# Optimization experiments

Hardware: AMD Instinct MI355X
Metric: run time of the kernel (lower is better)

## Reference

```python
import jax, jax.numpy as jnp
import numpy as np

B, T, V, Dm = 2, 2048, 32000, 1024
DI, N, R, L, K = 2048, 16, 64, 4, 4  # d_inner, n_states, dt_rank, n_layers, conv kernel


def setup_inputs() -> dict:
    key = jax.random.key(0)
    ks = jax.random.split(key, 10)
    ids = jax.random.randint(ks[0], (B, T), 0, V)

    def nrm(k, shape, s=0.02):
        return jax.random.normal(k, shape, jnp.float32) * s

    embed_W = nrm(ks[1], (V, Dm)).at[0].set(0.0)  # padding_idx=0 row zeroed; tied with output proj
    out_b = jnp.zeros((V,), jnp.float32)
    ln_w = jnp.ones((Dm,), jnp.float32)
    ln_b = jnp.zeros((Dm,), jnp.float32)
    norm_w = jnp.ones((L, Dm), jnp.float32)
    norm_b = jnp.zeros((L, Dm), jnp.float32)
    in_proj_W = nrm(ks[2], (L, 2 * DI, Dm))
    conv_W = nrm(ks[3], (L, DI, K), 0.1)
    conv_b = jnp.zeros((L, DI), jnp.float32)
    x_proj_W = nrm(ks[4], (L, R + 2 * N, DI))
    dt_proj_W = nrm(ks[5], (L, DI, R), 0.1)
    dt_proj_b = nrm(ks[6], (L, DI), 0.1)
    A_log = jnp.tile(jnp.log(jnp.arange(1, N + 1, dtype=jnp.float32)), (L, DI, 1))
    D_param = jnp.ones((L, DI), jnp.float32)
    out_proj_W = nrm(ks[7], (L, Dm, DI))
    return dict(ids=ids, embed_W=embed_W, out_b=out_b, ln_w=ln_w, ln_b=ln_b,
                norm_w=norm_w, norm_b=norm_b, in_proj_W=in_proj_W, conv_W=conv_W,
                conv_b=conv_b, x_proj_W=x_proj_W, dt_proj_W=dt_proj_W,
                dt_proj_b=dt_proj_b, A_log=A_log, D_param=D_param, out_proj_W=out_proj_W)


def layernorm(x, w, b, eps=1e-5):
    mu = x.mean(-1, keepdims=True)
    var = ((x - mu) ** 2).mean(-1, keepdims=True)
    return (x - mu) * jax.lax.rsqrt(var + eps) * w + b


def causal_dwconv(x, w, b):  # x [B,T,DI], w [DI,K], depthwise causal conv
    y = jax.lax.conv_general_dilated(
        x.transpose(0, 2, 1), w[:, None, :], (1,), [(K - 1, 0)],
        dimension_numbers=("NCH", "OIH", "NCH"), feature_group_count=DI)
    return y.transpose(0, 2, 1) + b


def selective_scan(u, dt, A, Bm, Cm, Dp):
    # u,dt [B,T,DI]; A [DI,N]; Bm,Cm [B,T,N]; Dp [DI]
    xs = (u.transpose(1, 0, 2), dt.transpose(1, 0, 2),
          Bm.transpose(1, 0, 2), Cm.transpose(1, 0, 2))

    def step(h, inp):
        u_t, dt_t, B_t, C_t = inp
        dA = jnp.exp(dt_t[..., None] * A)                     # [B,DI,N]
        h = dA * h + (dt_t * u_t)[..., None] * B_t[:, None, :]
        return h, (h * C_t[:, None, :]).sum(-1)               # y_t [B,DI]

    h0 = jnp.zeros((u.shape[0], DI, N), u.dtype)
    _, ys = jax.lax.scan(step, h0, xs)
    return ys.transpose(1, 0, 2) + u * Dp


def mamba_block(x, nw, nb, inW, cW, cb, xW, dtW, dtb, Alog, Dp, oW):
    res = x
    h = layernorm(x, nw, nb)
    xz = jnp.einsum("btd,ed->bte", h, inW)                    # [B,T,2*DI]
    x_in, z = xz[..., :DI], xz[..., DI:]
    xc = jax.nn.silu(causal_dwconv(x_in, cW, cb))
    proj = jnp.einsum("bte,pe->btp", xc, xW)                  # [B,T,R+2N]
    dt_r, Bm, Cm = proj[..., :R], proj[..., R:R + N], proj[..., R + N:]
    dt = jax.nn.softplus(jnp.einsum("btr,er->bte", dt_r, dtW) + dtb)
    A = -jnp.exp(Alog)
    y = selective_scan(xc, dt, A, Bm, Cm, Dp)
    y = y * jax.nn.silu(z)
    return res + jnp.einsum("bte,de->btd", y, oW)


def reference(ids, embed_W, out_b, ln_w, ln_b, norm_w, norm_b, in_proj_W, conv_W,
              conv_b, x_proj_W, dt_proj_W, dt_proj_b, A_log, D_param, out_proj_W):
    x = embed_W[ids]
    for l in range(L):
        x = mamba_block(x, norm_w[l], norm_b[l], in_proj_W[l], conv_W[l], conv_b[l],
                        x_proj_W[l], dt_proj_W[l], dt_proj_b[l], A_log[l],
                        D_param[l], out_proj_W[l])
    x = layernorm(x, ln_w, ln_b)
    return jnp.einsum("btd,vd->btv", x, embed_W) + out_b  # tied output projection
```

## Files before the change

kernel.cpp:

```cpp
#include <hip/hip_runtime.h>
#include <math.h>

#define B_   2
#define T_   2048
#define V_   32000
#define DM   1024
#define DI_  2048
#define NS   16
#define RR   64
#define LL   4
#define KK   4
#define BT   (B_*T_)

typedef unsigned short u16;
typedef unsigned int   u32;
typedef __attribute__((ext_vector_type(8))) short  bfrag;
typedef __attribute__((ext_vector_type(4))) float  f32x4;

__device__ __forceinline__ float siluf(float x){ return x / (1.0f + __expf(-x)); }
__device__ __forceinline__ float softplusf(float x){
    return (x > 20.0f) ? x : log1pf(__expf(x));
}

__device__ __forceinline__ u32 bf_rne(float f){
    u32 u = __float_as_uint(f);
    return (u + 0x7fffu + ((u >> 16) & 1u)) >> 16;
}
__device__ __forceinline__ void split4(const float4 v, uint2& hh, uint2& ll){
    u32 hx = __float_as_uint(v.x) >> 16;
    u32 hy = __float_as_uint(v.y) >> 16;
    u32 hz = __float_as_uint(v.z) >> 16;
    u32 hw = __float_as_uint(v.w) >> 16;
    hh.x = hx | (hy << 16);
    hh.y = hz | (hw << 16);
    float lx = v.x - __uint_as_float(hx << 16);
    float ly = v.y - __uint_as_float(hy << 16);
    float lz = v.z - __uint_as_float(hz << 16);
    float lw = v.w - __uint_as_float(hw << 16);
    ll.x = bf_rne(lx) | (bf_rne(ly) << 16);
    ll.y = bf_rne(lz) | (bf_rne(lw) << 16);
}
__device__ __forceinline__ void split1(float v, u16& h, u16& l){
    u32 hv = __float_as_uint(v) >> 16;
    h = (u16)hv;
    l = (u16)bf_rne(v - __uint_as_float(hv << 16));
}

__device__ __forceinline__ void gload16(const void* g, void* l){
    __builtin_amdgcn_global_load_lds(
        (const __attribute__((address_space(1))) unsigned int*)g,
        (__attribute__((address_space(3))) unsigned int*)l, 16, 0, 0);
}

__global__ __launch_bounds__(256) void embed_kernel(
    const int* __restrict__ ids, const float* __restrict__ W, float* __restrict__ x)
{
    int idx = blockIdx.x * 256 + threadIdx.x;
    int d  = idx & (DM - 1);
    int bt = idx >> 10;
    x[idx] = W[(size_t)ids[bt] * DM + d];
}

__global__ __launch_bounds__(256) void ln_kernel(
    const float* __restrict__ x, const float* __restrict__ w,
    const float* __restrict__ b, float* __restrict__ o,
    u16* __restrict__ oh, u16* __restrict__ ol)
{
    int row = blockIdx.x;
    const float4* xr = (const float4*)(x + (size_t)row * DM);
    float4 v = xr[threadIdx.x];
    float s = v.x + v.y + v.z + v.w;
    float q = v.x*v.x + v.y*v.y + v.z*v.z + v.w*v.w;
    #pragma unroll
    for (int off = 32; off > 0; off >>= 1) {
        s += __shfl_down(s, off);
        q += __shfl_down(q, off);
    }
    __shared__ float rs_[4], rq_[4];
    __shared__ float mu_s, inv_s;
    int lane = threadIdx.x & 63, wv = threadIdx.x >> 6;
    if (lane == 0) { rs_[wv] = s; rq_[wv] = q; }
    __syncthreads();
    if (threadIdx.x == 0) {
        float S = rs_[0] + rs_[1] + rs_[2] + rs_[3];
        float Q = rq_[0] + rq_[1] + rq_[2] + rq_[3];
        float mu  = S * (1.0f / DM);
        float var = Q * (1.0f / DM) - mu * mu;
        mu_s = mu; inv_s = rsqrtf(var + 1e-5f);
    }
    __syncthreads();
    float mu = mu_s, inv = inv_s;
    float4 wv4 = ((const float4*)w)[threadIdx.x];
    float4 bv4 = ((const float4*)b)[threadIdx.x];
    float4 r;
    r.x = (v.x - mu) * inv * wv4.x + bv4.x;
    r.y = (v.y - mu) * inv * wv4.y + bv4.y;
    r.z = (v.z - mu) * inv * wv4.z + bv4.z;
    r.w = (v.w - mu) * inv * wv4.w + bv4.w;
    if (o) ((float4*)(o + (size_t)row * DM))[threadIdx.x] = r;
    if (oh) {
        uint2 hh, ll; split4(r, hh, ll);
        ((uint2*)(oh + (size_t)row * DM))[threadIdx.x] = hh;
        ((uint2*)(ol + (size_t)row * DM))[threadIdx.x] = ll;
    }
}

__global__ __launch_bounds__(256) void conv_silu_kernel(
    const float* __restrict__ xz, const float* __restrict__ cw,
    const float* __restrict__ cb, float* __restrict__ xc,
    u16* __restrict__ xh, u16* __restrict__ xl)
{
    int idx = blockIdx.x * 256 + threadIdx.x;
    int c  = idx & (DI_ - 1);
    int bt = idx >> 11;
    int t  = bt & (T_ - 1);
    const float* base = xz + (size_t)bt * (2 * DI_) + c;
    float w0 = cw[c*KK+0], w1 = cw[c*KK+1], w2 = cw[c*KK+2], w3 = cw[c*KK+3];
    float acc = cb[c];
    if (t >= 3) acc += base[-3 * 2 * DI_] * w0;
    if (t >= 2) acc += base[-2 * 2 * DI_] * w1;
    if (t >= 1) acc += base[-1 * 2 * DI_] * w2;
    acc += base[0] * w3;
    float v = siluf(acc);
    xc[idx] = v;
    if (xh) { u16 h, l; split1(v, h, l); xh[idx] = h; xl[idx] = l; }
}

__global__ __launch_bounds__(256) void scan_kernel(
    const float* __restrict__ dt, int dt_stride,
    const float* __restrict__ u,
    const float* __restrict__ proj,
    const float* __restrict__ z, int z_stride,
    const float* __restrict__ A_log, const float* __restrict__ Dp,
    float* __restrict__ yf, u16* __restrict__ yh, u16* __restrict__ yl)
{
    int b   = blockIdx.x / (DI_ / 16);
    int di0 = (blockIdx.x % (DI_ / 16)) * 16;
    int tid = threadIdx.x;
    int ci = tid >> 4, n = tid & 15;
    int li = tid >> 4, lc = tid & 15;
    int di = di0 + ci;
    float Av = -__expf(A_log[di * NS + n]);
    float Dv = Dp[di];

    __shared__ float dt_s[16][16], u_s[16][16], Bs[16][16], Cs[16][16];
    __shared__ float ps[16][16][17];

    size_t bt0 = (size_t)b * T_ + li;
    float r_dt = dt[bt0 * dt_stride + di0 + lc];
    float r_u  = u[bt0 * DI_ + di0 + lc];
    float r_B  = proj[bt0 * (RR + 2*NS) + RR + lc];
    float r_C  = proj[bt0 * (RR + 2*NS) + RR + NS + lc];
    float r_z  = z[bt0 * z_stride + di0 + lc];

    float h = 0.0f;
    for (int t0 = 0; t0 < T_; t0 += 16) {
        dt_s[li][lc] = r_dt; u_s[li][lc] = r_u; Bs[li][lc] = r_B; Cs[li][lc] = r_C;
        float cz = r_z;
        if (t0 + 16 < T_) {
            size_t bt2 = (size_t)b * T_ + t0 + 16 + li;
            r_dt = dt[bt2 * dt_stride + di0 + lc];
            r_u  = u[bt2 * DI_ + di0 + lc];
            r_B  = proj[bt2 * (RR + 2*NS) + RR + lc];
            r_C  = proj[bt2 * (RR + 2*NS) + RR + NS + lc];
            r_z  = z[bt2 * z_stride + di0 + lc];
        }
        __syncthreads();
        #pragma unroll
        for (int i = 0; i < 16; i++) {
            float dtv = dt_s[i][ci];
            float uv  = u_s[i][ci];
            float dA  = __expf(dtv * Av);
            h = dA * h + dtv * uv * Bs[i][n];
            float p = h * Cs[i][n];
            if (n == 0) p += uv * Dv;
            ps[i][ci][n] = p;
        }
        __syncthreads();
        float s = 0.0f;
        #pragma unroll
        for (int k = 0; k < 16; k++) s += ps[li][lc][k];
        size_t bty = (size_t)b * T_ + t0 + li;
        float yv = s * siluf(cz);
        size_t oidx = bty * DI_ + di0 + lc;
        if (yf) yf[oidx] = yv;
        if (yh) { u16 hv, lv; split1(yv, hv, lv); yh[oidx] = hv; yl[oidx] = lv; }
    }
}

__global__ __launch_bounds__(256) void split_kernel(
    const float* __restrict__ src, u16* __restrict__ hi, u16* __restrict__ lo, int n4)
{
    int i = blockIdx.x * 256 + threadIdx.x;
    int stride = gridDim.x * 256;
    for (; i < n4; i += stride) {
        float4 v = ((const float4*)src)[i];
        uint2 hh, ll; split4(v, hh, ll);
        ((uint2*)hi)[i] = hh; ((uint2*)lo)[i] = ll;
    }
}

__global__ __launch_bounds__(256) void split_xw_kernel(
    const float* __restrict__ src, u16* __restrict__ hi, u16* __restrict__ lo)
{
    int idx = blockIdx.x * 256 + threadIdx.x;
    int l = idx >> 18;
    int rem = idx & 262143;
    int r = rem >> 11, cc = rem & 2047;
    float v = (r < 96) ? src[((size_t)l * 96 + r) * DI_ + cc] : 0.0f;
    u16 h, lo_; split1(v, h, lo_);
    hi[idx] = h; lo[idx] = lo_;
}

__global__ __launch_bounds__(256) void reduce_xproj(
    const float* __restrict__ part, float* __restrict__ proj,
    u16* __restrict__ ph, u16* __restrict__ pl)
{
    int idx = blockIdx.x * 256 + threadIdx.x;
    float s = 0.0f;
    #pragma unroll
    for (int k = 0; k < 8; k++) s += part[(size_t)k * BT * 96 + idx];
    proj[idx] = s;
    u16 h, l; split1(s, h, l); ph[idx] = h; pl[idx] = l;
}

template<int EPI, bool SPLITK>
__global__ __launch_bounds__(256) void gemm_bf3(
    const u16* __restrict__ Ah, const u16* __restrict__ Al, int lda,
    const u16* __restrict__ Bh, const u16* __restrict__ Bl, int ldb,
    float* __restrict__ C, int ldc,
    const float* __restrict__ bias,
    const float* __restrict__ Res, int ldres,
    int N, int Kd)
{
    __shared__ u16 lds[4][128][32];

    const int tid  = threadIdx.x;
    const int lane = tid & 63, wave = tid >> 6;
    const int m0 = blockIdx.y * 128;
    int n0, kbeg, kend;
    float* Cb = C;
    if (SPLITK) {
        n0 = 0;
        int KS = Kd >> 3;
        kbeg = blockIdx.x * KS; kend = kbeg + KS;
        Cb = C + (size_t)blockIdx.x * BT * 96;
    } else {
        n0 = blockIdx.x * 128; kbeg = 0; kend = Kd;
    }

    const int lr = lane & 15, lc = lane >> 4;
    const int rsw = (lr >> 1) & 3;
    const int wm = (wave >> 1) * 64, wn = (wave & 1) * 64;

    f32x4 acc[4][4];
    #pragma unroll
    for (int i = 0; i < 4; i++)
        #pragma unroll
        for (int j = 0; j < 4; j++)
            acc[i][j] = (f32x4){0.f, 0.f, 0.f, 0.f};

    const u16* mat = (wave == 0) ? Ah : (wave == 1) ? Al : (wave == 2) ? Bh : Bl;
    const size_t ldby = ((wave < 2) ? (size_t)lda : (size_t)ldb) * 2;
    const int r0 = (wave < 2) ? m0 : n0;
    const char* gsrc = (const char*)mat + (size_t)(r0 + (lane >> 2)) * ldby
                     + ((((lane & 3) ^ ((lane >> 3) & 3))) << 4);

    for (int k0 = kbeg; k0 < kend; k0 += 32) {
        const char* g = gsrc + (size_t)k0 * 2;
        #pragma unroll
        for (int c = 0; c < 8; c++)
            gload16(g + (size_t)c * 16 * ldby, (void*)&lds[wave][c * 16][0]);
        __syncthreads();

        const int cs = (lc ^ rsw) * 8;
        bfrag afh[4], bfh[4];
        #pragma unroll
        for (int i = 0; i < 4; i++) {
            afh[i] = *(const bfrag*)&lds[0][wm + i*16 + lr][cs];
            bfh[i] = *(const bfrag*)&lds[2][wn + i*16 + lr][cs];
        }
        #pragma unroll
        for (int i = 0; i < 4; i++)
            #pragma unroll
            for (int j = 0; j < 4; j++)
                acc[i][j] = __builtin_amdgcn_mfma_f32_16x16x32_bf16(afh[i], bfh[j], acc[i][j], 0, 0, 0);
        bfrag afl[4];
        #pragma unroll
        for (int i = 0; i < 4; i++)
            afl[i] = *(const bfrag*)&lds[1][wm + i*16 + lr][cs];
        #pragma unroll
        for (int i = 0; i < 4; i++)
            #pragma unroll
            for (int j = 0; j < 4; j++)
                acc[i][j] = __builtin_amdgcn_mfma_f32_16x16x32_bf16(afl[i], bfh[j], acc[i][j], 0, 0, 0);
        bfrag bfl[4];
        #pragma unroll
        for (int i = 0; i < 4; i++)
            bfl[i] = *(const bfrag*)&lds[3][wn + i*16 + lr][cs];
        #pragma unroll
        for (int i = 0; i < 4; i++)
            #pragma unroll
            for (int j = 0; j < 4; j++)
                acc[i][j] = __builtin_amdgcn_mfma_f32_16x16x32_bf16(afh[i], bfl[j], acc[i][j], 0, 0, 0);
        __syncthreads();
    }

    #pragma unroll
    for (int j = 0; j < 4; j++) {
        int nn = n0 + wn + j*16 + lr;
        if (nn < N) {
            float bs = (EPI & 1) ? bias[nn] : 0.f;
            #pragma unroll
            for (int i = 0; i < 4; i++) {
                #pragma unroll
                for (int r = 0; r < 4; r++) {
                    int m = m0 + wm + i*16 + lc*4 + r;
                    float v = acc[i][j][r];
                    if (EPI & 1) v += bs;
                    if (EPI & 2) v = softplusf(v);
                    if (EPI & 4) v += Res[(size_t)m * ldres + nn];
                    Cb[(size_t)m * ldc + nn] = v;
                }
            }
        }
    }
}

template<int EPI, bool NG>
__global__ __launch_bounds__(256) void gemm_nt_mfma(
    const float* __restrict__ A, int lda,
    const float* __restrict__ Bm, int ldb,
    float* __restrict__ C, int ldc,
    const float* __restrict__ bias,
    const float* __restrict__ Res, int ldres,
    int N, int Kd)
{
    __shared__ __align__(16) u16 lds[4][128][40];
    const int tid  = threadIdx.x;
    const int m0   = blockIdx.y * 128, n0 = blockIdx.x * 128;
    const int lane = tid & 63, wave = tid >> 6;
    const int wm   = (wave >> 1) * 64, wn = (wave & 1) * 64;
    const int lr   = lane & 15, lc = lane >> 4;
    f32x4 acc[4][4];
    #pragma unroll
    for (int i = 0; i < 4; i++)
        #pragma unroll
        for (int j = 0; j < 4; j++)
            acc[i][j] = (f32x4){0.f, 0.f, 0.f, 0.f};
    const float* Ab = A  + (size_t)m0 * lda;
    const float* Bb = Bm + (size_t)n0 * ldb;
    for (int k0 = 0; k0 < Kd; k0 += 32) {
        uint2 ahh[4], alo[4], bhh[4], blo[4];
        #pragma unroll
        for (int i = 0; i < 4; i++) {
            int idx = tid + i * 256;
            int r = idx >> 3, c = (idx & 7) << 2;
            float4 av = *(const float4*)(Ab + (size_t)r * lda + k0 + c);
            float4 bv;
            if (!NG || (n0 + r) < N)
                bv = *(const float4*)(Bb + (size_t)r * ldb + k0 + c);
            else
                bv = make_float4(0.f,0.f,0.f,0.f);
            split4(av, ahh[i], alo[i]);
            split4(bv, bhh[i], blo[i]);
        }
        __syncthreads();
        #pragma unroll
        for (int i = 0; i < 4; i++) {
            int idx = tid + i * 256;
            int r = idx >> 3, c = (idx & 7) << 2;
            *(uint2*)&lds[0][r][c] = ahh[i];
            *(uint2*)&lds[1][r][c] = alo[i];
            *(uint2*)&lds[2][r][c] = bhh[i];
            *(uint2*)&lds[3][r][c] = blo[i];
        }
        __syncthreads();
        bfrag afh[4], afl[4], bfh[4], bfl[4];
        #pragma unroll
        for (int i = 0; i < 4; i++) {
            afh[i] = *(const bfrag*)&lds[0][wm + i*16 + lr][lc*8];
            afl[i] = *(const bfrag*)&lds[1][wm + i*16 + lr][lc*8];
            bfh[i] = *(const bfrag*)&lds[2][wn + i*16 + lr][lc*8];
            bfl[i] = *(const bfrag*)&lds[3][wn + i*16 + lr][lc*8];
        }
        #pragma unroll
        for (int i = 0; i < 4; i++)
            #pragma unroll
            for (int j = 0; j < 4; j++) {
                f32x4 a = acc[i][j];
                a = __builtin_amdgcn_mfma_f32_16x16x32_bf16(afh[i], bfh[j], a, 0, 0, 0);
                a = __builtin_amdgcn_mfma_f32_16x16x32_bf16(afl[i], bfh[j], a, 0, 0, 0);
                a = __builtin_amdgcn_mfma_f32_16x16x32_bf16(afh[i], bfl[j], a, 0, 0, 0);
                acc[i][j] = a;
            }
    }
    #pragma unroll
    for (int j = 0; j < 4; j++) {
        int n = n0 + wn + j*16 + lr;
        if (NG && n >= N) continue;
        float bs = (EPI & 1) ? bias[n] : 0.f;
        #pragma unroll
        for (int i = 0; i < 4; i++) {
            #pragma unroll
            for (int r = 0; r < 4; r++) {
                int m = m0 + wm + i*16 + lc*4 + r;
                float v = acc[i][j][r];
                if (EPI & 1) v += bs;
                if (EPI & 2) v = softplusf(v);
                if (EPI & 4) v += Res[(size_t)m * ldres + n];
                C[(size_t)m * ldc + n] = v;
            }
        }
    }
}

extern "C" void kernel_launch(void* const* d_in, const int* in_sizes, int n_in,
                              void* d_out, int out_size, void* d_ws, size_t ws_size,
                              hipStream_t stream)
{
    const int*   ids    = (const int*)  d_in[0];
    const float* embedW = (const float*)d_in[1];
    const float* out_b  = (const float*)d_in[2];
    const float* ln_w   = (const float*)d_in[3];
    const float* ln_b   = (const float*)d_in[4];
    const float* norm_w = (const float*)d_in[5];
    const float* norm_b = (const float*)d_in[6];
    const float* inW    = (const float*)d_in[7];
    const float* convW  = (const float*)d_in[8];
    const float* convB  = (const float*)d_in[9];
    const float* xW     = (const float*)d_in[10];
    const float* dtW    = (const float*)d_in[11];
    const float* dtB    = (const float*)d_in[12];
    const float* Alog   = (const float*)d_in[13];
    const float* Dp     = (const float*)d_in[14];
    const float* oW     = (const float*)d_in[15];
    float* logits = (float*)d_out;

    const size_t fX  = (size_t)BT * DM;
    const size_t fXZ = (size_t)BT * 2 * DI_;
    const size_t fXC = (size_t)BT * DI_;
    const size_t fPJ = (size_t)BT * 96;
    float* x    = (float*)d_ws;
    float* xz   = x    + fX;
    float* xc   = xz   + fXZ;
    float* proj = xc   + fXC;
    float* part = proj + fPJ;
    u16* p16 = (u16*)(part + 8 * fPJ);
    u16* hh  = p16; p16 += fX;   u16* hl  = p16; p16 += fX;
    u16* xch = p16; p16 += fXC;  u16* xcl = p16; p16 += fXC;
    u16* pjh = p16; p16 += fPJ;  u16* pjl = p16; p16 += fPJ;
    const size_t winW = (size_t)LL * 2 * DI_ * DM;
    u16* inWh = p16; p16 += winW; u16* inWl = p16; p16 += winW;
    const size_t wxW = (size_t)LL * 128 * DI_;
    u16* xWh = p16; p16 += wxW;  u16* xWl = p16; p16 += wxW;
    const size_t wdtW = (size_t)LL * DI_ * RR;
    u16* dtWh = p16; p16 += wdtW; u16* dtWl = p16; p16 += wdtW;
    const size_t woW = (size_t)LL * DM * DI_;
    u16* oWh = p16; p16 += woW;  u16* oWl = p16; p16 += woW;
    const size_t weW = (size_t)V_ * DM;
    u16* eWh = p16; p16 += weW;  u16* eWl = p16; p16 += weW;
    const size_t NEED = (size_t)((char*)p16 - (char*)d_ws);

    if (ws_size < NEED) {
        float* fx    = (float*)d_ws;
        float* fh    = fx + fX;
        float* fxz   = fh + fX;
        float* fxc   = fxz + fXZ;
        float* fproj = fxc + fXC;
        embed_kernel<<<BT*DM/256, 256, 0, stream>>>(ids, embedW, fx);
        for (int l = 0; l < LL; l++) {
            ln_kernel<<<BT, 256, 0, stream>>>(fx, norm_w + (size_t)l*DM, norm_b + (size_t)l*DM, fh, nullptr, nullptr);
            gemm_nt_mfma<0, false><<<dim3(32, 32), 256, 0, stream>>>(
                fh, DM, inW + (size_t)l*2*DI_*DM, DM, fxz, 2*DI_, nullptr, nullptr, 0, 2*DI_, DM);
            conv_silu_kernel<<<BT*DI_/256, 256, 0, stream>>>(
                fxz, convW + (size_t)l*DI_*KK, convB + (size_t)l*DI_, fxc, nullptr, nullptr);
            gemm_nt_mfma<0, true><<<dim3(1, 32), 256, 0, stream>>>(
                fxc, DI_, xW + (size_t)l*(RR+2*NS)*DI_, DI_, fproj, RR+2*NS, nullptr, nullptr, 0, RR+2*NS, DI_);
            gemm_nt_mfma<3, false><<<dim3(16, 32), 256, 0, stream>>>(
                fproj, RR+2*NS, dtW + (size_t)l*DI_*RR, RR, fxz, 2*DI_, dtB + (size_t)l*DI_, nullptr, 0, DI_, RR);
            scan_kernel<<<B_*(DI_/16), 256, 0, stream>>>(
                fxz, 2*DI_, fxc, fproj, fxz + DI_, 2*DI_,
                Alog + (size_t)l*DI_*NS, Dp + (size_t)l*DI_, fxc, nullptr, nullptr);
            gemm_nt_mfma<4, false><<<dim3(8, 32), 256, 0, stream>>>(
                fxc, DI_, oW + (size_t)l*DM*DI_, DI_, fx, DM, nullptr, fx, DM, DM, DI_);
        }
        ln_kernel<<<BT, 256, 0, stream>>>(fx, ln_w, ln_b, fh, nullptr, nullptr);
        gemm_nt_mfma<1, false><<<dim3(V_/128, 32), 256, 0, stream>>>(
            fh, DM, embedW, DM, logits, V_, out_b, nullptr, 0, V_, DM);
        return;
    }

    split_kernel<<<4096, 256, 0, stream>>>(inW, inWh, inWl, (int)(winW / 4));
    split_kernel<<<2048, 256, 0, stream>>>(dtW, dtWh, dtWl, (int)(wdtW / 4));
    split_kernel<<<4096, 256, 0, stream>>>(oW, oWh, oWl, (int)(woW / 4));
    split_kernel<<<8192, 256, 0, stream>>>(embedW, eWh, eWl, (int)(weW / 4));
    split_xw_kernel<<<4096, 256, 0, stream>>>(xW, xWh, xWl);

    embed_kernel<<<BT*DM/256, 256, 0, stream>>>(ids, embedW, x);

    for (int l = 0; l < LL; l++) {
        ln_kernel<<<BT, 256, 0, stream>>>(x, norm_w + (size_t)l*DM, norm_b + (size_t)l*DM,
                                          nullptr, hh, hl);
        gemm_bf3<0, false><<<dim3(32, 32), 256, 0, stream>>>(
            hh, hl, DM, inWh + l*2*DI_*DM, inWl + l*2*DI_*DM, DM,
            xz, 2*DI_, nullptr, nullptr, 0, 2*DI_, DM);
        conv_silu_kernel<<<BT*DI_/256, 256, 0, stream>>>(
            xz, convW + (size_t)l*DI_*KK, convB + (size_t)l*DI_, xc, xch, xcl);
        gemm_bf3<0, true><<<dim3(8, 32), 256, 0, stream>>>(
            xch, xcl, DI_, xWh + l*128*DI_, xWl + l*128*DI_, DI_,
            part, 96, nullptr, nullptr, 0, 96, DI_);
        reduce_xproj<<<BT*96/256, 256, 0, stream>>>(part, proj, pjh, pjl);
        gemm_bf3<3, false><<<dim3(16, 32), 256, 0, stream>>>(
            pjh, pjl, 96, dtWh + l*DI_*RR, dtWl + l*DI_*RR, RR,
            xz, 2*DI_, dtB + (size_t)l*DI_, nullptr, 0, DI_, RR);
        scan_kernel<<<B_*(DI_/16), 256, 0, stream>>>(
            xz, 2*DI_, xc, proj, xz + DI_, 2*DI_,
            Alog + (size_t)l*DI_*NS, Dp + (size_t)l*DI_, nullptr, xch, xcl);
        gemm_bf3<4, false><<<dim3(8, 32), 256, 0, stream>>>(
            xch, xcl, DI_, oWh + l*DM*DI_, oWl + l*DM*DI_, DI_,
            x, DM, nullptr, x, DM, DM, DI_);
    }

    ln_kernel<<<BT, 256, 0, stream>>>(x, ln_w, ln_b, nullptr, hh, hl);
    gemm_bf3<1, false><<<dim3(V_/128, 32), 256, 0, stream>>>(
        hh, hl, DM, eWh, eWl, DM, logits, V_, out_b, nullptr, 0, V_, DM);
}
```

Before: 3.423 ms.

## Double-buffer LDS tiles in bf16x3 GEMM and swizzle workgroups for logits GEMM

The split-bf16 GEMM now keeps two LDS stages, issuing async global loads for the next K-slice before computing on the current one. It waits with an explicit vmcnt and raw s_barrier rather than __syncthreads, so memory latency overlaps the MFMA work. The large vocab projection also remaps workgroup IDs across XCD-sized groups to improve L2 locality. LDS use doubles, which may lower occupancy, and the hand-written waitcnt counts depend on each wave issuing exactly 8 loads per stage.

Measured after the change: 3.103 ms. 9.4% less time.

```diff
diff --git a/kernel.cpp b/kernel.cpp
--- a/kernel.cpp
+++ b/kernel.cpp
@@ -224,7 +224,7 @@
     u16 h, l; split1(s, h, l); ph[idx] = h; pl[idx] = l;
 }
 
-template<int EPI, bool SPLITK>
+template<int EPI, bool SPLITK, bool SWZ>
 __global__ __launch_bounds__(256) void gemm_bf3(
     const u16* __restrict__ Ah, const u16* __restrict__ Al, int lda,
     const u16* __restrict__ Bh, const u16* __restrict__ Bl, int ldb,
@@ -233,20 +233,29 @@
     const float* __restrict__ Res, int ldres,
     int N, int Kd)
 {
-    __shared__ u16 lds[4][128][32];
+    __shared__ __align__(16) u16 lds[2][4][128][32];
+
+    int bx = blockIdx.x, by = blockIdx.y;
+    if (SWZ) {
+        int gx = gridDim.x;
+        int nwg = gx * gridDim.y;
+        int lid = by * gx + bx;
+        int s = (lid & 7) * (nwg >> 3) + (lid >> 3);
+        bx = s % gx; by = s / gx;
+    }
 
     const int tid  = threadIdx.x;
     const int lane = tid & 63, wave = tid >> 6;
-    const int m0 = blockIdx.y * 128;
+    const int m0 = by * 128;
     int n0, kbeg, kend;
     float* Cb = C;
     if (SPLITK) {
         n0 = 0;
         int KS = Kd >> 3;
-        kbeg = blockIdx.x * KS; kend = kbeg + KS;
-        Cb = C + (size_t)blockIdx.x * BT * 96;
+        kbeg = bx * KS; kend = kbeg + KS;
+        Cb = C + (size_t)bx * BT * 96;
     } else {
-        n0 = blockIdx.x * 128; kbeg = 0; kend = Kd;
+        n0 = bx * 128; kbeg = 0; kend = Kd;
     }
 
     const int lr = lane & 15, lc = lane >> 4;
@@ -266,19 +275,34 @@
     const char* gsrc = (const char*)mat + (size_t)(r0 + (lane >> 2)) * ldby
                      + ((((lane & 3) ^ ((lane >> 3) & 3))) << 4);
 
+    {
+        const char* g = gsrc + (size_t)kbeg * 2;
+        #pragma unroll
+        for (int c = 0; c < 8; c++)
+            gload16(g + (size_t)c * 16 * ldby, (void*)&lds[0][wave][c * 16][0]);
+    }
+
+    int cur = 0;
     for (int k0 = kbeg; k0 < kend; k0 += 32) {
-        const char* g = gsrc + (size_t)k0 * 2;
-        #pragma unroll
-        for (int c = 0; c < 8; c++)
-            gload16(g + (size_t)c * 16 * ldby, (void*)&lds[wave][c * 16][0]);
-        __syncthreads();
+        const bool pf = (k0 + 32 < kend);
+        if (pf) {
+            const char* g = gsrc + (size_t)(k0 + 32) * 2;
+            #pragma unroll
+            for (int c = 0; c < 8; c++)
+                gload16(g + (size_t)c * 16 * ldby, (void*)&lds[cur ^ 1][wave][c * 16][0]);
+        }
+        __builtin_amdgcn_sched_barrier(0);
+        if (pf) asm volatile("s_waitcnt vmcnt(8)" ::: "memory");
+        else    asm volatile("s_waitcnt vmcnt(0)" ::: "memory");
+        __builtin_amdgcn_s_barrier();
+        __builtin_amdgcn_sched_barrier(0);
 
         const int cs = (lc ^ rsw) * 8;
         bfrag afh[4], bfh[4];
         #pragma unroll
         for (int i = 0; i < 4; i++) {
-            afh[i] = *(const bfrag*)&lds[0][wm + i*16 + lr][cs];
-            bfh[i] = *(const bfrag*)&lds[2][wn + i*16 + lr][cs];
+            afh[i] = *(const bfrag*)&lds[cur][0][wm + i*16 + lr][cs];
+            bfh[i] = *(const bfrag*)&lds[cur][2][wn + i*16 + lr][cs];
         }
         #pragma unroll
         for (int i = 0; i < 4; i++)
@@ -288,7 +312,7 @@
         bfrag afl[4];
         #pragma unroll
         for (int i = 0; i < 4; i++)
-            afl[i] = *(const bfrag*)&lds[1][wm + i*16 + lr][cs];
+            afl[i] = *(const bfrag*)&lds[cur][1][wm + i*16 + lr][cs];
         #pragma unroll
         for (int i = 0; i < 4; i++)
             #pragma unroll
@@ -297,13 +321,17 @@
         bfrag bfl[4];
         #pragma unroll
         for (int i = 0; i < 4; i++)
-            bfl[i] = *(const bfrag*)&lds[3][wn + i*16 + lr][cs];
+            bfl[i] = *(const bfrag*)&lds[cur][3][wn + i*16 + lr][cs];
         #pragma unroll
         for (int i = 0; i < 4; i++)
             #pragma unroll
             for (int j = 0; j < 4; j++)
                 acc[i][j] = __builtin_amdgcn_mfma_f32_16x16x32_bf16(afh[i], bfl[j], acc[i][j], 0, 0, 0);
-        __syncthreads();
+
+        asm volatile("s_waitcnt lgkmcnt(0)" ::: "memory");
+        __builtin_amdgcn_s_barrier();
+        __builtin_amdgcn_sched_barrier(0);
+        cur ^= 1;
     }
 
     #pragma unroll
@@ -502,27 +530,27 @@
     for (int l = 0; l < LL; l++) {
         ln_kernel<<<BT, 256, 0, stream>>>(x, norm_w + (size_t)l*DM, norm_b + (size_t)l*DM,
                                           nullptr, hh, hl);
-        gemm_bf3<0, false><<<dim3(32, 32), 256, 0, stream>>>(
+        gemm_bf3<0, false, false><<<dim3(32, 32), 256, 0, stream>>>(
             hh, hl, DM, inWh + l*2*DI_*DM, inWl + l*2*DI_*DM, DM,
             xz, 2*DI_, nullptr, nullptr, 0, 2*DI_, DM);
         conv_silu_kernel<<<BT*DI_/256, 256, 0, stream>>>(
             xz, convW + (size_t)l*DI_*KK, convB + (size_t)l*DI_, xc, xch, xcl);
-        gemm_bf3<0, true><<<dim3(8, 32), 256, 0, stream>>>(
+        gemm_bf3<0, true, false><<<dim3(8, 32), 256, 0, stream>>>(
             xch, xcl, DI_, xWh + l*128*DI_, xWl + l*128*DI_, DI_,
             part, 96, nullptr, nullptr, 0, 96, DI_);
         reduce_xproj<<<BT*96/256, 256, 0, stream>>>(part, proj, pjh, pjl);
-        gemm_bf3<3, false><<<dim3(16, 32), 256, 0, stream>>>(
+        gemm_bf3<3, false, false><<<dim3(16, 32), 256, 0, stream>>>(
             pjh, pjl, 96, dtWh + l*DI_*RR, dtWl + l*DI_*RR, RR,
             xz, 2*DI_, dtB + (size_t)l*DI_, nullptr, 0, DI_, RR);
         scan_kernel<<<B_*(DI_/16), 256, 0, stream>>>(
             xz, 2*DI_, xc, proj, xz + DI_, 2*DI_,
             Alog + (size_t)l*DI_*NS, Dp + (size_t)l*DI_, nullptr, xch, xcl);
-        gemm_bf3<4, false><<<dim3(8, 32), 256, 0, stream>>>(
+        gemm_bf3<4, false, false><<<dim3(8, 32), 256, 0, stream>>>(
             xch, xcl, DI_, oWh + l*DM*DI_, oWl + l*DM*DI_, DI_,
             x, DM, nullptr, x, DM, DM, DI_);
     }
 
     ln_kernel<<<BT, 256, 0, stream>>>(x, ln_w, ln_b, nullptr, hh, hl);
-    gemm_bf3<1, false><<<dim3(V_/128, 32), 256, 0, stream>>>(
+    gemm_bf3<1, false, true><<<dim3(V_/128, 32), 256, 0, stream>>>(
         hh, hl, DM, eWh, eWl, DM, logits, V_, out_b, nullptr, 0, V_, DM);
 }
```
